# Optimization experiments

Hardware: AMD Instinct MI355X
Metric: run time of the kernel (lower is better)

The kernel has to match this reference:

```python
import jax, jax.numpy as jnp
import numpy as np
from jax import lax

D_MODEL = 1024
N_HEADS = 16
D_STATE = 1024
D_INNER = 1024
D_CONV = 4
CHUNK = 64
BATCH = 2
SEQ = 4096
CONV_DIM = 2 * D_STATE + D_INNER  # 3072
D_IN_PROJ = CONV_DIM + N_HEADS    # 3088


def segsum(a):
    """a: [..., T] -> [..., T, T] segment-sum: out[i,j] = sum_{j<k<=i} a[k], -inf above diag."""
    T = a.shape[-1]
    idx = jnp.arange(T)
    strict = idx[:, None] > idx[None, :]          # i > j
    xx = jnp.where(strict, a[..., :, None], 0.0)  # broadcast a along new last (e) dim
    s = jnp.cumsum(xx, axis=-2)
    incl = idx[:, None] >= idx[None, :]
    return jnp.where(incl, s, -jnp.inf)


def ssd(xv, A, Bm, Cm, l):
    """Mamba-2 SSD chunked scan with max-normalized decays and norm denominator.
    xv:[b,S,h,p] A:[b,S,h] Bm:[b,S,h,n] Cm:[b,S,h,n]"""
    b, S, h, p = xv.shape
    n = Bm.shape[-1]
    c = S // l
    xv = xv.reshape(b, c, l, h, p)
    A = A.reshape(b, c, l, h)
    Bm = Bm.reshape(b, c, l, h, n)
    Cm = Cm.reshape(b, c, l, h, n)
    A = jnp.transpose(A, (0, 3, 1, 2))                  # b h c l
    A_cumsum = jnp.cumsum(A, axis=-1)                   # b h c l
    L_log = segsum(A)                                   # b h c l l
    L = jnp.exp(L_log - jnp.max(L_log, axis=-1, keepdims=True))
    norm_diag = jnp.transpose(L.sum(-1), (0, 2, 3, 1))  # b c l h
    Y_diag = jnp.einsum('bclhn,bcshn,bhcls,bcshp->bclhp', Cm, Bm, L, xv)
    decay_states = A_cumsum[..., -1:] - A_cumsum        # b h c l
    decay_states = jnp.exp(decay_states - jnp.max(decay_states, axis=-1, keepdims=True))
    norm_decay = jnp.transpose(decay_states.sum(-1), (0, 2, 1))  # b c h
    states = jnp.einsum('bclhn,bhcl,bclhp->bchpn', Bm, decay_states, xv)
    norm_decay = jnp.pad(norm_decay, ((0, 0), (1, 0), (0, 0)))
    states = jnp.pad(states, ((0, 0), (1, 0), (0, 0), (0, 0), (0, 0)))
    A_last = jnp.pad(A_cumsum[..., -1], ((0, 0), (0, 0), (1, 0)))  # b h c+1
    decay_chunk = segsum(A_last)                        # b h c+1 c+1
    decay_chunk = jnp.exp(decay_chunk - jnp.max(decay_chunk, axis=-1, keepdims=True))
    norm_decay = jnp.einsum('bhzc,bch->bzh', decay_chunk, norm_decay)[:, :-1]  # b c h
    states = jnp.einsum('bhzc,bchpn->bzhpn', decay_chunk, states)[:, :-1]      # b c h p n
    state_decay_out = jnp.exp(A_cumsum - jnp.max(A_cumsum, axis=-1, keepdims=True))
    norm_off = jnp.einsum('bch,bhcl->bclh', norm_decay, state_decay_out)
    Y_off = jnp.einsum('bclhn,bchpn,bhcl->bclhp', Cm, states, state_decay_out)
    Y = (Y_diag + Y_off).reshape(b, S, h, p)
    norm = (norm_diag + norm_off).reshape(b, S, h)
    return Y / norm[..., None]


def setup_inputs() -> dict:
    key = jax.random.key(0)
    ks = jax.random.split(key, 6)
    x = jax.random.normal(ks[0], (BATCH, SEQ, D_MODEL), dtype=jnp.float32)
    in_proj_w = jax.random.normal(ks[1], (D_IN_PROJ, D_MODEL), dtype=jnp.float32) * 0.02
    conv_w = jax.random.normal(ks[2], (CONV_DIM, 1, D_CONV), dtype=jnp.float32) * 0.3
    conv_b = jnp.zeros((CONV_DIM,), dtype=jnp.float32)
    w_base = jax.random.uniform(ks[3], (N_HEADS,), dtype=jnp.float32, minval=-0.5, maxval=0.5)
    out_proj_w = jax.random.normal(ks[4], (D_MODEL, D_INNER), dtype=jnp.float32) * 0.02
    return {"x": x, "in_proj_w": in_proj_w, "conv_w": conv_w, "conv_b": conv_b,
            "w_base": w_base, "out_proj_w": out_proj_w}


def reference(x, in_proj_w, conv_w, conv_b, w_base, out_proj_w):
    b, S, _ = x.shape  # S divisible by CHUNK -> no padding branch
    xIOw = x @ in_proj_w.T                                  # [b,S,3088]
    xIO, w = xIOw[..., :CONV_DIM], xIOw[..., CONV_DIM:]
    # causal depthwise conv1d (pad d_conv-1 on both sides, keep first S == left pad)
    y = lax.conv_general_dilated(
        jnp.transpose(xIO, (0, 2, 1)), conv_w, window_strides=(1,),
        padding=[(D_CONV - 1, 0)], feature_group_count=CONV_DIM,
        dimension_numbers=('NCH', 'OIH', 'NCH'))
    xIO = jnp.transpose(y + conv_b[None, :, None], (0, 2, 1))  # [b,S,3072]
    xs = xIO[..., :D_STATE].reshape(b, S, N_HEADS, D_STATE // N_HEADS)
    I = xIO[..., D_STATE:2 * D_STATE].reshape(b, S, N_HEADS, D_STATE // N_HEADS)
    O = xIO[..., 2 * D_STATE:].reshape(b, S, N_HEADS, D_INNER // N_HEADS)
    w = w * w_base                                          # [b,S,h]
    out = ssd(O, w, I, xs, CHUNK)                           # [b,S,h,p]
    out = out.reshape(b, S, D_INNER) @ out_proj_w.T
    return out[:, :S]
```

## Files before the change

kernel.cpp:

```cpp
#include <hip/hip_runtime.h>
#include <hip/hip_bf16.h>
#include <math.h>
#include <stdint.h>

#define SEQL 4096
#define NH 16
#define CDIM 3072
#define DPROJ 3088
#define DMODEL 1024

typedef __bf16 nbf16;
typedef __attribute__((ext_vector_type(8))) __bf16 bf16x8;
typedef __attribute__((ext_vector_type(4))) float f32x4;

__device__ inline void store_val(float* p, float v) { *p = v; }
__device__ inline void store_val(nbf16* p, float v) { *p = (nbf16)v; }

__device__ __forceinline__ void gload_lds16(const void* g, void* l) {
  __builtin_amdgcn_global_load_lds(
      (const __attribute__((address_space(1))) void*)g,
      (__attribute__((address_space(3))) void*)l, 16, 0, 0);
}

__device__ __forceinline__ int swz(int row, int col) {
  return row * 64 + (col ^ ((row & 7) << 3));
}

template <typename TOUT>
__global__ __launch_bounds__(256) void gemm_mfma(const nbf16* __restrict__ A,
                                                 const nbf16* __restrict__ B,
                                                 TOUT* __restrict__ C,
                                                 int M, int N, int K) {
  __shared__ __align__(16) nbf16 Alds[2][128 * 64];
  __shared__ __align__(16) nbf16 Blds[2][128 * 64];
  int tid = threadIdx.x;
  int lane = tid & 63;
  int w = tid >> 6, wm = w >> 1, wn = w & 1;
  int gx = gridDim.x;
  int nwg = gx * gridDim.y;
  int orig = blockIdx.y * gx + blockIdx.x;
  int wg = (orig & 7) * (nwg >> 3) + (orig >> 3);
  int bm = (wg / gx) * 128, bn = (wg % gx) * 128;
  const nbf16* Ag = A + (size_t)bm * K;
  const nbf16* Bg = B + (size_t)bn * K;
  f32x4 acc[4][4] = {};
  const int nt = K >> 6;

  auto STAGE = [&](int buf, int k0) {
#pragma unroll
    for (int q = 0; q < 4; ++q) {
      int e = (q * 256 + tid) * 8;
      int row = e >> 6;
      int cs = (e >> 3) & 7;
      int sc = (cs ^ (row & 7)) << 3;
      gload_lds16(Ag + (size_t)row * K + k0 + sc, &Alds[buf][e]);
      gload_lds16(Bg + (size_t)row * K + k0 + sc, &Blds[buf][e]);
    }
  };
  auto COMPUTE = [&](int buf) {
#pragma unroll
    for (int kk = 0; kk < 64; kk += 32) {
      bf16x8 af[4], bfr[4];
      int col = kk + (lane >> 4) * 8;
#pragma unroll
      for (int i = 0; i < 4; ++i) {
        af[i]  = *(const bf16x8*)&Alds[buf][swz(wm * 64 + i * 16 + (lane & 15), col)];
        bfr[i] = *(const bf16x8*)&Blds[buf][swz(wn * 64 + i * 16 + (lane & 15), col)];
      }
#pragma unroll
      for (int mi = 0; mi < 4; ++mi)
#pragma unroll
        for (int ni = 0; ni < 4; ++ni)
          acc[mi][ni] = __builtin_amdgcn_mfma_f32_16x16x32_bf16(af[mi], bfr[ni], acc[mi][ni], 0, 0, 0);
    }
  };

  STAGE(0, 0);
  asm volatile("s_waitcnt vmcnt(0)" ::: "memory");
  __builtin_amdgcn_s_barrier();
  for (int t = 0; t < nt - 1; ++t) {
    int cur = t & 1;
    STAGE(cur ^ 1, (t + 1) << 6);
    COMPUTE(cur);
    asm volatile("s_waitcnt vmcnt(0)" ::: "memory");
    __builtin_amdgcn_s_barrier();
  }
  COMPUTE((nt - 1) & 1);

#pragma unroll
  for (int mi = 0; mi < 4; ++mi)
#pragma unroll
    for (int ni = 0; ni < 4; ++ni) {
      int colw = bn + wn * 64 + ni * 16 + (lane & 15);
      if (colw >= N) continue;
#pragma unroll
      for (int j = 0; j < 4; ++j) {
        int roww = bm + wm * 64 + mi * 16 + (lane >> 4) * 4 + j;
        store_val(&C[(size_t)roww * N + colw], acc[mi][ni][j]);
      }
    }
}

__global__ __launch_bounds__(256) void cast_bf16(const float* __restrict__ in,
                                                 nbf16* __restrict__ out, long n) {
  long i = ((long)blockIdx.x * 256 + threadIdx.x) * 4;
  if (i >= n) return;
  float4 v = *(const float4*)(in + i);
  out[i] = (nbf16)v.x; out[i + 1] = (nbf16)v.y;
  out[i + 2] = (nbf16)v.z; out[i + 3] = (nbf16)v.w;
}

__global__ __launch_bounds__(256) void cast_pad_w(const float* __restrict__ in,
                                                  nbf16* __restrict__ out) {
  long i = ((long)blockIdx.x * 256 + threadIdx.x) * 4;
  if (i >= (long)3200 * 1024) return;
  int row = (int)(i >> 10);
  if (row < DPROJ) {
    float4 v = *(const float4*)(in + i);
    out[i] = (nbf16)v.x; out[i + 1] = (nbf16)v.y;
    out[i + 2] = (nbf16)v.z; out[i + 3] = (nbf16)v.w;
  } else {
    out[i] = (nbf16)0.f; out[i + 1] = (nbf16)0.f;
    out[i + 2] = (nbf16)0.f; out[i + 3] = (nbf16)0.f;
  }
}

__global__ __launch_bounds__(256) void ssd_intra(
    const nbf16* __restrict__ xw, const float* __restrict__ cw,
    const float* __restrict__ cb, const float* __restrict__ wbase,
    nbf16* __restrict__ Ydg, nbf16* __restrict__ stG,
    float* __restrict__ norm_diag, float* __restrict__ sdo_g,
    float* __restrict__ ndecay, float* __restrict__ Alast) {
  __shared__ __align__(16) nbf16 Craw[68 * 64];
  __shared__ __align__(16) nbf16 Braw[68 * 64];
  __shared__ __align__(16) nbf16 Xraw[68 * 64];
  __shared__ __align__(16) nbf16 BbT[64 * 64];
  __shared__ __align__(16) nbf16 XbT[64 * 64];
  __shared__ float cums_s[64], mincs_s[64], dec_s[64];
  nbf16* Sb = Xraw;

  int tid = threadIdx.x;
  int lane = tid & 63;
  int w = tid >> 6;
  int h = blockIdx.x & 15;
  int c = (blockIdx.x >> 4) & 63;
  int b = blockIdx.x >> 10;

  for (int i = tid; i < 67 * 8; i += 256) {
    int row = i >> 3, n0 = (i & 7) * 8;
    int t = c * 64 - 3 + row;
    bf16x8 vc = {}, vb = {}, vx = {};
    if (t >= 0) {
      const nbf16* r = xw + ((size_t)(b * SEQL + t)) * DPROJ + h * 64 + n0;
      vc = *(const bf16x8*)(r);
      vb = *(const bf16x8*)(r + 1024);
      vx = *(const bf16x8*)(r + 2048);
    }
    int idx = swz(row, n0);
    *(bf16x8*)&Craw[idx] = vc;
    *(bf16x8*)&Braw[idx] = vb;
    *(bf16x8*)&Xraw[idx] = vx;
  }

  if (w == 0) {
    float a = (float)xw[((size_t)(b * SEQL + c * 64 + lane)) * DPROJ + CDIM + h] * wbase[h];
    float cum = a;
#pragma unroll
    for (int d = 1; d < 64; d <<= 1) {
      float t = __shfl_up(cum, d, 64);
      if (lane >= d) cum += t;
    }
    float mn = cum;
#pragma unroll
    for (int d = 1; d < 64; d <<= 1) {
      float t = __shfl_up(mn, d, 64);
      if (lane >= d) mn = fminf(mn, t);
    }
    float mnall = __shfl(mn, 63, 64);
    float mx = cum;
#pragma unroll
    for (int d = 1; d < 64; d <<= 1) mx = fmaxf(mx, __shfl_xor(mx, d, 64));
    float dec = expf(mnall - cum);
    float sdo = expf(cum - mx);
    float nd = dec;
#pragma unroll
    for (int d = 1; d < 64; d <<= 1) nd += __shfl_xor(nd, d, 64);
    cums_s[lane] = cum; mincs_s[lane] = mn; dec_s[lane] = dec;
    sdo_g[(size_t)blockIdx.x * 64 + lane] = sdo;
    if (lane == 0) ndecay[blockIdx.x] = nd;
    if (lane == 63) Alast[((size_t)(b * NH + h)) * 64 + c] = cum;
  }
  __syncthreads();

  float rc[16], rb[16], rx[16];
  {
    int n = tid & 63, base = tid >> 6;
    const float* wcc = cw + (size_t)(h * 64 + n) * 4;
    const float* wcb = wcc + 4096;
    const float* wcx = wcc + 8192;
    float bcc = cb[h * 64 + n], bcb = cb[1024 + h * 64 + n], bcx = cb[2048 + h * 64 + n];
#pragma unroll
    for (int q = 0; q < 16; ++q) {
      int l = base + q * 4;
      float aC = bcc, aB = bcb, aX = bcx;
#pragma unroll
      for (int d = 0; d < 4; ++d) {
        int idx = swz(l + d, n);
        aC = fmaf((float)Craw[idx], wcc[d], aC);
        aB = fmaf((float)Braw[idx], wcb[d], aB);
        aX = fmaf((float)Xraw[idx], wcx[d], aX);
      }
      rc[q] = aC; rb[q] = aB; rx[q] = aX;
    }
  }
  __syncthreads();
  {
    int n = tid & 63, base = tid >> 6;
#pragma unroll
    for (int q = 0; q < 16; ++q) {
      int l = base + q * 4;
      Craw[swz(l, n)] = (nbf16)rc[q];
      Braw[swz(l, n)] = (nbf16)rb[q];
      BbT[swz(n, l)] = (nbf16)rb[q];
      XbT[swz(n, l)] = (nbf16)rx[q];
    }
  }
  __syncthreads();

  {
    f32x4 accS[4] = {};
#pragma unroll
    for (int kk = 0; kk < 64; kk += 32) {
      int arow = w * 16 + (lane & 15);
      int c0 = kk + (lane >> 4) * 8;
      bf16x8 af = *(const bf16x8*)&Craw[swz(arow, c0)];
#pragma unroll
      for (int nb = 0; nb < 4; ++nb) {
        int brow = nb * 16 + (lane & 15);
        bf16x8 bfr = *(const bf16x8*)&Braw[swz(brow, c0)];
        accS[nb] = __builtin_amdgcn_mfma_f32_16x16x32_bf16(af, bfr, accS[nb], 0, 0, 0);
      }
    }
    float rowsum[4] = {0.f, 0.f, 0.f, 0.f};
#pragma unroll
    for (int nb = 0; nb < 4; ++nb) {
      int s = nb * 16 + (lane & 15);
      float cs = cums_s[s];
#pragma unroll
      for (int r = 0; r < 4; ++r) {
        int l = w * 16 + (lane >> 4) * 4 + r;
        float e = (s <= l) ? expf(mincs_s[l] - cs) : 0.f;
        rowsum[r] += e;
        Sb[swz(l, s)] = (nbf16)(accS[nb][r] * e);
      }
    }
#pragma unroll
    for (int r = 0; r < 4; ++r) {
#pragma unroll
      for (int d = 1; d < 16; d <<= 1) rowsum[r] += __shfl_xor(rowsum[r], d, 64);
      if ((lane & 15) == 0) {
        int l = w * 16 + (lane >> 4) * 4 + r;
        norm_diag[(size_t)blockIdx.x * 64 + l] = rowsum[r];
      }
    }
  }
  __syncthreads();

  {
    f32x4 accY[4] = {};
#pragma unroll
    for (int kk = 0; kk < 64; kk += 32) {
      int arow = w * 16 + (lane & 15);
      int c0 = kk + (lane >> 4) * 8;
      bf16x8 af = *(const bf16x8*)&Sb[swz(arow, c0)];
#pragma unroll
      for (int pb = 0; pb < 4; ++pb) {
        int prow = pb * 16 + (lane & 15);
        bf16x8 bfr = *(const bf16x8*)&XbT[swz(prow, c0)];
        accY[pb] = __builtin_amdgcn_mfma_f32_16x16x32_bf16(af, bfr, accY[pb], 0, 0, 0);
      }
    }
    size_t ybase = ((size_t)(b * SEQL + c * 64)) * DMODEL + h * 64;
#pragma unroll
    for (int pb = 0; pb < 4; ++pb) {
      int p = pb * 16 + (lane & 15);
#pragma unroll
      for (int r = 0; r < 4; ++r) {
        int l = w * 16 + (lane >> 4) * 4 + r;
        Ydg[ybase + (size_t)l * DMODEL + p] = (nbf16)accY[pb][r];
      }
    }
  }

  {
    f32x4 accT[4] = {};
#pragma unroll
    for (int kk = 0; kk < 64; kk += 32) {
      int prow = w * 16 + (lane & 15);
      int c0 = kk + (lane >> 4) * 8;
      bf16x8 xf = *(const bf16x8*)&XbT[swz(prow, c0)];
      bf16x8 af;
#pragma unroll
      for (int j = 0; j < 8; ++j) af[j] = (nbf16)((float)xf[j] * dec_s[c0 + j]);
#pragma unroll
      for (int nb = 0; nb < 4; ++nb) {
        int nrow = nb * 16 + (lane & 15);
        bf16x8 bfr = *(const bf16x8*)&BbT[swz(nrow, c0)];
        accT[nb] = __builtin_amdgcn_mfma_f32_16x16x32_bf16(af, bfr, accT[nb], 0, 0, 0);
      }
    }
    size_t sbase = (((size_t)(b * NH + h)) * 64 + c) * 4096;
#pragma unroll
    for (int nb = 0; nb < 4; ++nb) {
      int n = nb * 16 + (lane & 15);
#pragma unroll
      for (int r = 0; r < 4; ++r) {
        int p = w * 16 + (lane >> 4) * 4 + r;
        stG[sbase + p * 64 + n] = (nbf16)accT[nb][r];
      }
    }
  }
}

__global__ __launch_bounds__(256) void ssd_scan(
    const float* __restrict__ Alast, const nbf16* __restrict__ stG,
    const float* __restrict__ ndecay, nbf16* __restrict__ siG,
    float* __restrict__ nd_in) {
  __shared__ __align__(16) nbf16 Msw[64 * 64];
  __shared__ __align__(16) nbf16 StT[256 * 64];
  __shared__ float Qs[66], mzS[64];
  int tid = threadIdx.x, lane = tid & 63, w = tid >> 6;
  int et = blockIdx.x & 15, h = (blockIdx.x >> 4) & 15, b = blockIdx.x >> 8;

  if (w == 0) {
    float a = Alast[((size_t)(b * NH + h)) * 64 + lane];
    float s = a;
#pragma unroll
    for (int d = 1; d < 64; d <<= 1) {
      float t = __shfl_up(s, d, 64);
      if (lane >= d) s += t;
    }
    float Q = __shfl_up(s, 1, 64);
    if (lane == 0) Q = 0.f;
    float m = Q;
#pragma unroll
    for (int d = 1; d < 64; d <<= 1) {
      float t = __shfl_up(m, d, 64);
      if (lane >= d) m = fminf(m, t);
    }
    Qs[lane] = Q; mzS[lane] = m;
    if (lane == 0) { Qs[64] = 0.f; Qs[65] = 0.f; }
  }
  __syncthreads();

#pragma unroll
  for (int k = 0; k < 16; ++k) {
    int i = tid + (k << 8);
    int z = i >> 6, j = i & 63;
    float v = (j < z) ? expf(mzS[z] - Qs[j + 1]) : 0.f;
    Msw[swz(z, j)] = (nbf16)v;
  }
  size_t stbase = ((size_t)(b * NH + h)) * 64 * 4096 + et * 256;
#pragma unroll
  for (int q = 0; q < 8; ++q) {
    int i = tid + (q << 8);
    int cc = i >> 5, oct = i & 31;
    bf16x8 v = *(const bf16x8*)&stG[stbase + (size_t)cc * 4096 + oct * 8];
#pragma unroll
    for (int jj = 0; jj < 8; ++jj) StT[swz(oct * 8 + jj, cc)] = v[jj];
  }
  __syncthreads();

  if (et == 0 && tid < 64) {
    int z = tid;
    float acc = 0.f;
    for (int j = 0; j < z; ++j)
      acc += expf(mzS[z] - Qs[j + 1]) * ndecay[((size_t)(b * 64 + j)) * 16 + h];
    nd_in[((size_t)(b * 64 + z)) * 16 + h] = acc;
  }

  f32x4 acc[4][4] = {};
#pragma unroll
  for (int kk = 0; kk < 64; kk += 32) {
    int c0 = kk + (lane >> 4) * 8;
    bf16x8 af[4], bfr[4];
#pragma unroll
    for (int i = 0; i < 4; ++i) {
      af[i]  = *(const bf16x8*)&Msw[swz(i * 16 + (lane & 15), c0)];
      bfr[i] = *(const bf16x8*)&StT[swz(w * 64 + i * 16 + (lane & 15), c0)];
    }
#pragma unroll
    for (int mi = 0; mi < 4; ++mi)
#pragma unroll
      for (int ni = 0; ni < 4; ++ni)
        acc[mi][ni] = __builtin_amdgcn_mfma_f32_16x16x32_bf16(af[mi], bfr[ni], acc[mi][ni], 0, 0, 0);
  }
  size_t obase = ((size_t)(b * NH + h)) * 64 * 4096 + et * 256;
#pragma unroll
  for (int mi = 0; mi < 4; ++mi)
#pragma unroll
    for (int ni = 0; ni < 4; ++ni) {
      int e = w * 64 + ni * 16 + (lane & 15);
#pragma unroll
      for (int r = 0; r < 4; ++r) {
        int z = mi * 16 + (lane >> 4) * 4 + r;
        siG[obase + (size_t)z * 4096 + e] = (nbf16)acc[mi][ni][r];
      }
    }
}

__global__ __launch_bounds__(256) void ssd_off(
    const nbf16* __restrict__ xw, const float* __restrict__ cw,
    const float* __restrict__ cb, const nbf16* __restrict__ siG,
    const float* __restrict__ norm_diag, const float* __restrict__ sdo_g,
    const float* __restrict__ nd_in, nbf16* __restrict__ Ydg) {
  __shared__ __align__(16) nbf16 Craw[68 * 64];
  __shared__ __align__(16) nbf16 Ssb[64 * 64];
  int tid = threadIdx.x, lane = tid & 63, w = tid >> 6;
  int h = blockIdx.x & 15, c = (blockIdx.x >> 4) & 63, b = blockIdx.x >> 10;

  for (int i = tid; i < 67 * 8; i += 256) {
    int row = i >> 3, n0 = (i & 7) * 8;
    int t = c * 64 - 3 + row;
    bf16x8 v = {};
    if (t >= 0) v = *(const bf16x8*)(xw + ((size_t)(b * SEQL + t)) * DPROJ + h * 64 + n0);
    *(bf16x8*)&Craw[swz(row, n0)] = v;
  }
  {
    size_t sbase = (((size_t)(b * NH + h)) * 64 + c) * 4096;
    for (int i = tid; i < 512; i += 256) {
      int p = i >> 3, n0 = (i & 7) * 8;
      bf16x8 v = *(const bf16x8*)&siG[sbase + p * 64 + n0];
      *(bf16x8*)&Ssb[swz(p, n0)] = v;
    }
  }
  __syncthreads();

  float rc[16];
  {
    int n = tid & 63, base = tid >> 6;
    const float* wcc = cw + (size_t)(h * 64 + n) * 4;
    float bcc = cb[h * 64 + n];
#pragma unroll
    for (int q = 0; q < 16; ++q) {
      int l = base + q * 4;
      float aC = bcc;
#pragma unroll
      for (int d = 0; d < 4; ++d) aC = fmaf((float)Craw[swz(l + d, n)], wcc[d], aC);
      rc[q] = aC;
    }
  }
  __syncthreads();
  {
    int n = tid & 63, base = tid >> 6;
#pragma unroll
    for (int q = 0; q < 16; ++q) Craw[swz(base + q * 4, n)] = (nbf16)rc[q];
  }
  __syncthreads();

  f32x4 accO[4] = {};
#pragma unroll
  for (int kk = 0; kk < 64; kk += 32) {
    int arow = w * 16 + (lane & 15);
    int c0 = kk + (lane >> 4) * 8;
    bf16x8 af = *(const bf16x8*)&Craw[swz(arow, c0)];
#pragma unroll
    for (int pb = 0; pb < 4; ++pb) {
      int prow = pb * 16 + (lane & 15);
      bf16x8 bfr = *(const bf16x8*)&Ssb[swz(prow, c0)];
      accO[pb] = __builtin_amdgcn_mfma_f32_16x16x32_bf16(af, bfr, accO[pb], 0, 0, 0);
    }
  }
  float ndin = nd_in[blockIdx.x];
  size_t ybase = ((size_t)(b * SEQL + c * 64)) * DMODEL + h * 64;
#pragma unroll
  for (int r = 0; r < 4; ++r) {
    int l = w * 16 + (lane >> 4) * 4 + r;
    float sd = sdo_g[(size_t)blockIdx.x * 64 + l];
    float nrm = norm_diag[(size_t)blockIdx.x * 64 + l] + ndin * sd;
#pragma unroll
    for (int pb = 0; pb < 4; ++pb) {
      int p = pb * 16 + (lane & 15);
      size_t yi = ybase + (size_t)l * DMODEL + p;
      Ydg[yi] = (nbf16)(((float)Ydg[yi] + accO[pb][r] * sd) / nrm);
    }
  }
}

extern "C" void kernel_launch(void* const* d_in, const int* in_sizes, int n_in,
                              void* d_out, int out_size, void* d_ws, size_t ws_size,
                              hipStream_t stream) {
  const float* x          = (const float*)d_in[0];
  const float* in_proj_w  = (const float*)d_in[1];
  const float* conv_w     = (const float*)d_in[2];
  const float* conv_b     = (const float*)d_in[3];
  const float* w_base     = (const float*)d_in[4];
  const float* out_proj_w = (const float*)d_in[5];
  float* out = (float*)d_out;

  char* ws = (char*)d_ws;
  size_t off = 0;
  auto alloc = [&](size_t bytes) {
    void* p = ws + off;
    off += (bytes + 255) & ~(size_t)255;
    return p;
  };
  const size_t BT = (size_t)2 * SEQL;
  nbf16* xIOw = (nbf16*)alloc(BT * DPROJ * 2);
  nbf16* xbf  = (nbf16*)alloc(BT * DMODEL * 2);
  nbf16* wibf = (nbf16*)alloc((size_t)3200 * 1024 * 2);
  nbf16* wobf = (nbf16*)alloc((size_t)1024 * 1024 * 2);
  nbf16* stG  = (nbf16*)alloc((size_t)2048 * 4096 * 2);
  nbf16* siG  = (nbf16*)alloc((size_t)2048 * 4096 * 2);
  float* norm_diag = (float*)alloc((size_t)2048 * 64 * 4);
  float* sdo   = (float*)alloc((size_t)2048 * 64 * 4);
  float* ndec  = (float*)alloc((size_t)2048 * 4);
  float* Alast = (float*)alloc((size_t)2048 * 4);
  float* nd_in = (float*)alloc((size_t)2048 * 4);
  nbf16* Ydg = xbf;

  cast_bf16<<<(int)(BT * DMODEL / 4 / 256), 256, 0, stream>>>(x, xbf, BT * DMODEL);
  cast_pad_w<<<3200 * 1024 / 4 / 256, 256, 0, stream>>>(in_proj_w, wibf);
  cast_bf16<<<DMODEL * DMODEL / 4 / 256, 256, 0, stream>>>(out_proj_w, wobf, (long)DMODEL * DMODEL);
  gemm_mfma<nbf16><<<dim3(25, BT / 128), 256, 0, stream>>>(
      xbf, wibf, xIOw, (int)BT, DPROJ, DMODEL);
  ssd_intra<<<2048, 256, 0, stream>>>(xIOw, conv_w, conv_b, w_base,
                                      Ydg, stG, norm_diag, sdo, ndec, Alast);
  ssd_scan<<<512, 256, 0, stream>>>(Alast, stG, ndec, siG, nd_in);
  ssd_off<<<2048, 256, 0, stream>>>(xIOw, conv_w, conv_b, siG,
                                    norm_diag, sdo, nd_in, Ydg);
  gemm_mfma<float><<<dim3(DMODEL / 128, BT / 128), 256, 0, stream>>>(
      Ydg, wobf, out, (int)BT, DMODEL, DMODEL);
}
```

Before: 291.0 us.

## Deepen GEMM pipeline to 4 stages and cache convolved C for offdiag pass

The GEMM now uses a 4-buffer, K=32 tile pipeline with three loads in flight, partial vmcnt waits, and raised wave priority around the MFMA block. This is meant to hide global-load latency better than the old double buffer with a full drain each iteration. Separately, ssd_intra writes the convolved C values to a new buffer so ssd_off no longer reloads the raw projection and recomputes the depthwise conv. ssd_scan also writes its results in place into stG, removing the siG buffer. The trade-off is an extra global write and read of C, plus in-place scan writes that depend on how blocks partition the buffer.

```diff
diff --git a/kernel.cpp b/kernel.cpp
--- a/kernel.cpp
+++ b/kernel.cpp
@@ -25,14 +25,17 @@
 __device__ __forceinline__ int swz(int row, int col) {
   return row * 64 + (col ^ ((row & 7) << 3));
 }
+__device__ __forceinline__ int swz32(int row, int col) {
+  return row * 32 + (col ^ (((row >> 1) & 3) << 3));
+}
 
 template <typename TOUT>
 __global__ __launch_bounds__(256) void gemm_mfma(const nbf16* __restrict__ A,
                                                  const nbf16* __restrict__ B,
                                                  TOUT* __restrict__ C,
                                                  int M, int N, int K) {
-  __shared__ __align__(16) nbf16 Alds[2][128 * 64];
-  __shared__ __align__(16) nbf16 Blds[2][128 * 64];
+  __shared__ __align__(16) nbf16 Alds[4][128 * 32];
+  __shared__ __align__(16) nbf16 Blds[4][128 * 32];
   int tid = threadIdx.x;
   int lane = tid & 63;
   int w = tid >> 6, wm = w >> 1, wn = w & 1;
@@ -44,48 +47,52 @@
   const nbf16* Ag = A + (size_t)bm * K;
   const nbf16* Bg = B + (size_t)bn * K;
   f32x4 acc[4][4] = {};
-  const int nt = K >> 6;
-
-  auto STAGE = [&](int buf, int k0) {
-#pragma unroll
-    for (int q = 0; q < 4; ++q) {
+  const int nt = K >> 5;
+
+  auto STAGE = [&](int buf, int t) {
+#pragma unroll
+    for (int q = 0; q < 2; ++q) {
       int e = (q * 256 + tid) * 8;
-      int row = e >> 6;
-      int cs = (e >> 3) & 7;
-      int sc = (cs ^ (row & 7)) << 3;
-      gload_lds16(Ag + (size_t)row * K + k0 + sc, &Alds[buf][e]);
-      gload_lds16(Bg + (size_t)row * K + k0 + sc, &Blds[buf][e]);
+      int row = e >> 5;
+      int col = e & 31;
+      int sc = col ^ (((row >> 1) & 3) << 3);
+      gload_lds16(Ag + (size_t)row * K + t * 32 + sc, &Alds[buf][e]);
+      gload_lds16(Bg + (size_t)row * K + t * 32 + sc, &Blds[buf][e]);
     }
   };
   auto COMPUTE = [&](int buf) {
-#pragma unroll
-    for (int kk = 0; kk < 64; kk += 32) {
-      bf16x8 af[4], bfr[4];
-      int col = kk + (lane >> 4) * 8;
-#pragma unroll
-      for (int i = 0; i < 4; ++i) {
-        af[i]  = *(const bf16x8*)&Alds[buf][swz(wm * 64 + i * 16 + (lane & 15), col)];
-        bfr[i] = *(const bf16x8*)&Blds[buf][swz(wn * 64 + i * 16 + (lane & 15), col)];
-      }
-#pragma unroll
-      for (int mi = 0; mi < 4; ++mi)
-#pragma unroll
-        for (int ni = 0; ni < 4; ++ni)
-          acc[mi][ni] = __builtin_amdgcn_mfma_f32_16x16x32_bf16(af[mi], bfr[ni], acc[mi][ni], 0, 0, 0);
-    }
+    bf16x8 af[4], bfr[4];
+    int c0 = (lane >> 4) * 8;
+#pragma unroll
+    for (int i = 0; i < 4; ++i) {
+      af[i]  = *(const bf16x8*)&Alds[buf][swz32(wm * 64 + i * 16 + (lane & 15), c0)];
+      bfr[i] = *(const bf16x8*)&Blds[buf][swz32(wn * 64 + i * 16 + (lane & 15), c0)];
+    }
+    __builtin_amdgcn_s_setprio(1);
+#pragma unroll
+    for (int mi = 0; mi < 4; ++mi)
+#pragma unroll
+      for (int ni = 0; ni < 4; ++ni)
+        acc[mi][ni] = __builtin_amdgcn_mfma_f32_16x16x32_bf16(af[mi], bfr[ni], acc[mi][ni], 0, 0, 0);
+    __builtin_amdgcn_s_setprio(0);
   };
 
   STAGE(0, 0);
-  asm volatile("s_waitcnt vmcnt(0)" ::: "memory");
-  __builtin_amdgcn_s_barrier();
-  for (int t = 0; t < nt - 1; ++t) {
-    int cur = t & 1;
-    STAGE(cur ^ 1, (t + 1) << 6);
-    COMPUTE(cur);
-    asm volatile("s_waitcnt vmcnt(0)" ::: "memory");
+  STAGE(1, 1);
+  STAGE(2, 2);
+  for (int t = 0; t < nt; ++t) {
+    if (t + 3 < nt) STAGE((t + 3) & 3, t + 3);
+    int ahead = nt - 1 - t;
+    if (ahead >= 3)      asm volatile("s_waitcnt vmcnt(12)" ::: "memory");
+    else if (ahead == 2) asm volatile("s_waitcnt vmcnt(8)" ::: "memory");
+    else if (ahead == 1) asm volatile("s_waitcnt vmcnt(4)" ::: "memory");
+    else                 asm volatile("s_waitcnt vmcnt(0)" ::: "memory");
+    __builtin_amdgcn_sched_barrier(0);
     __builtin_amdgcn_s_barrier();
-  }
-  COMPUTE((nt - 1) & 1);
+    COMPUTE(t & 3);
+    __builtin_amdgcn_sched_barrier(0);
+    __builtin_amdgcn_s_barrier();
+  }
 
 #pragma unroll
   for (int mi = 0; mi < 4; ++mi)
@@ -129,6 +136,7 @@
     const nbf16* __restrict__ xw, const float* __restrict__ cw,
     const float* __restrict__ cb, const float* __restrict__ wbase,
     nbf16* __restrict__ Ydg, nbf16* __restrict__ stG,
+    nbf16* __restrict__ Ccv,
     float* __restrict__ norm_diag, float* __restrict__ sdo_g,
     float* __restrict__ ndecay, float* __restrict__ Alast) {
   __shared__ __align__(16) nbf16 Craw[68 * 64];
@@ -219,10 +227,12 @@
 #pragma unroll
     for (int q = 0; q < 16; ++q) {
       int l = base + q * 4;
-      Craw[swz(l, n)] = (nbf16)rc[q];
+      nbf16 cv = (nbf16)rc[q];
+      Craw[swz(l, n)] = cv;
       Braw[swz(l, n)] = (nbf16)rb[q];
       BbT[swz(n, l)] = (nbf16)rb[q];
       XbT[swz(n, l)] = (nbf16)rx[q];
+      Ccv[((size_t)(b * SEQL + c * 64 + l)) * DMODEL + h * 64 + n] = cv;
     }
   }
   __syncthreads();
@@ -323,9 +333,8 @@
 }
 
 __global__ __launch_bounds__(256) void ssd_scan(
-    const float* __restrict__ Alast, const nbf16* __restrict__ stG,
-    const float* __restrict__ ndecay, nbf16* __restrict__ siG,
-    float* __restrict__ nd_in) {
+    const float* __restrict__ Alast, nbf16* __restrict__ stG,
+    const float* __restrict__ ndecay, float* __restrict__ nd_in) {
   __shared__ __align__(16) nbf16 Msw[64 * 64];
   __shared__ __align__(16) nbf16 StT[256 * 64];
   __shared__ float Qs[66], mzS[64];
@@ -395,7 +404,7 @@
       for (int ni = 0; ni < 4; ++ni)
         acc[mi][ni] = __builtin_amdgcn_mfma_f32_16x16x32_bf16(af[mi], bfr[ni], acc[mi][ni], 0, 0, 0);
   }
-  size_t obase = ((size_t)(b * NH + h)) * 64 * 4096 + et * 256;
+  size_t obase = stbase;
 #pragma unroll
   for (int mi = 0; mi < 4; ++mi)
 #pragma unroll
@@ -404,27 +413,24 @@
 #pragma unroll
       for (int r = 0; r < 4; ++r) {
         int z = mi * 16 + (lane >> 4) * 4 + r;
-        siG[obase + (size_t)z * 4096 + e] = (nbf16)acc[mi][ni][r];
+        stG[obase + (size_t)z * 4096 + e] = (nbf16)acc[mi][ni][r];
       }
     }
 }
 
 __global__ __launch_bounds__(256) void ssd_off(
-    const nbf16* __restrict__ xw, const float* __restrict__ cw,
-    const float* __restrict__ cb, const nbf16* __restrict__ siG,
+    const nbf16* __restrict__ Ccv, const nbf16* __restrict__ siG,
     const float* __restrict__ norm_diag, const float* __restrict__ sdo_g,
     const float* __restrict__ nd_in, nbf16* __restrict__ Ydg) {
-  __shared__ __align__(16) nbf16 Craw[68 * 64];
+  __shared__ __align__(16) nbf16 Csw[64 * 64];
   __shared__ __align__(16) nbf16 Ssb[64 * 64];
   int tid = threadIdx.x, lane = tid & 63, w = tid >> 6;
   int h = blockIdx.x & 15, c = (blockIdx.x >> 4) & 63, b = blockIdx.x >> 10;
 
-  for (int i = tid; i < 67 * 8; i += 256) {
+  for (int i = tid; i < 512; i += 256) {
     int row = i >> 3, n0 = (i & 7) * 8;
-    int t = c * 64 - 3 + row;
-    bf16x8 v = {};
-    if (t >= 0) v = *(const bf16x8*)(xw + ((size_t)(b * SEQL + t)) * DPROJ + h * 64 + n0);
-    *(bf16x8*)&Craw[swz(row, n0)] = v;
+    bf16x8 v = *(const bf16x8*)&Ccv[((size_t)(b * SEQL + c * 64 + row)) * DMODEL + h * 64 + n0];
+    *(bf16x8*)&Csw[swz(row, n0)] = v;
   }
   {
     size_t sbase = (((size_t)(b * NH + h)) * 64 + c) * 4096;
@@ -436,34 +442,12 @@
   }
   __syncthreads();
 
-  float rc[16];
-  {
-    int n = tid & 63, base = tid >> 6;
-    const float* wcc = cw + (size_t)(h * 64 + n) * 4;
-    float bcc = cb[h * 64 + n];
-#pragma unroll
-    for (int q = 0; q < 16; ++q) {
-      int l = base + q * 4;
-      float aC = bcc;
-#pragma unroll
-      for (int d = 0; d < 4; ++d) aC = fmaf((float)Craw[swz(l + d, n)], wcc[d], aC);
-      rc[q] = aC;
-    }
-  }
-  __syncthreads();
-  {
-    int n = tid & 63, base = tid >> 6;
-#pragma unroll
-    for (int q = 0; q < 16; ++q) Craw[swz(base + q * 4, n)] = (nbf16)rc[q];
-  }
-  __syncthreads();
-
   f32x4 accO[4] = {};
 #pragma unroll
   for (int kk = 0; kk < 64; kk += 32) {
     int arow = w * 16 + (lane & 15);
     int c0 = kk + (lane >> 4) * 8;
-    bf16x8 af = *(const bf16x8*)&Craw[swz(arow, c0)];
+    bf16x8 af = *(const bf16x8*)&Csw[swz(arow, c0)];
 #pragma unroll
     for (int pb = 0; pb < 4; ++pb) {
       int prow = pb * 16 + (lane & 15);
@@ -511,7 +495,7 @@
   nbf16* wibf = (nbf16*)alloc((size_t)3200 * 1024 * 2);
   nbf16* wobf = (nbf16*)alloc((size_t)1024 * 1024 * 2);
   nbf16* stG  = (nbf16*)alloc((size_t)2048 * 4096 * 2);
-  nbf16* siG  = (nbf16*)alloc((size_t)2048 * 4096 * 2);
+  nbf16* Ccv  = (nbf16*)alloc(BT * DMODEL * 2);
   float* norm_diag = (float*)alloc((size_t)2048 * 64 * 4);
   float* sdo   = (float*)alloc((size_t)2048 * 64 * 4);
   float* ndec  = (float*)alloc((size_t)2048 * 4);
@@ -525,10 +509,9 @@
   gemm_mfma<nbf16><<<dim3(25, BT / 128), 256, 0, stream>>>(
       xbf, wibf, xIOw, (int)BT, DPROJ, DMODEL);
   ssd_intra<<<2048, 256, 0, stream>>>(xIOw, conv_w, conv_b, w_base,
-                                      Ydg, stG, norm_diag, sdo, ndec, Alast);
-  ssd_scan<<<512, 256, 0, stream>>>(Alast, stG, ndec, siG, nd_in);
-  ssd_off<<<2048, 256, 0, stream>>>(xIOw, conv_w, conv_b, siG,
-                                    norm_diag, sdo, nd_in, Ydg);
+                                      Ydg, stG, Ccv, norm_diag, sdo, ndec, Alast);
+  ssd_scan<<<512, 256, 0, stream>>>(Alast, stG, ndec, nd_in);
+  ssd_off<<<2048, 256, 0, stream>>>(Ccv, stG, norm_diag, sdo, nd_in, Ydg);
   gemm_mfma<float><<<dim3(DMODEL / 128, BT / 128), 256, 0, stream>>>(
       Ydg, wobf, out, (int)BT, DMODEL, DMODEL);
 }
```

New measurement: 301.4 us. 3.6% more time.
